# Kernel tuning notes

Hardware: AMD Instinct MI355X
Metric: run time of the kernel (lower is better)

## Reference

```python
import jax, jax.numpy as jnp
import numpy as np

B, P, ENC = 64, 196, 2048
H, A, E, V, T = 512, 512, 512, 10000, 20


def setup_inputs() -> dict:
    key = jax.random.key(0)
    ks = jax.random.split(key, 24)
    s = 0.02
    inp = {
        "encoder_out": jax.random.normal(ks[0], (B, P, ENC), jnp.float32),
        "captions": jax.random.randint(ks[1], (B, T), 0, V),
        "lengths": jnp.sort(jax.random.randint(ks[2], (B,), 5, T + 1))[::-1].at[0].set(T).astype(jnp.int32),
        # Attention
        "enc_att_w": jax.random.normal(ks[3], (A, ENC)) * s,
        "enc_att_b": jnp.zeros((A,)),
        "hid_att_w": jax.random.normal(ks[4], (A, H)) * s,
        "hid_att_b": jnp.zeros((A,)),
        "full_att_w": jax.random.normal(ks[5], (1, A)) * s,
        "full_att_b": jnp.zeros((1,)),
        # Embedding
        "embed_w": jax.random.uniform(ks[6], (V, E), minval=-0.1, maxval=0.1),
        # LSTMCell (input = embed + encoder -> E + ENC)
        "lstm_w_ih": jax.random.normal(ks[7], (4 * H, E + ENC)) * s,
        "lstm_w_hh": jax.random.normal(ks[8], (4 * H, H)) * s,
        "lstm_b_ih": jnp.zeros((4 * H,)),
        "lstm_b_hh": jnp.zeros((4 * H,)),
        # init hidden/cell from mean encoder features
        "init_h_w": jax.random.normal(ks[9], (H, ENC)) * s,
        "init_h_b": jnp.zeros((H,)),
        "init_c_w": jax.random.normal(ks[10], (H, ENC)) * s,
        "init_c_b": jnp.zeros((H,)),
        # gating
        "fbeta_w": jax.random.normal(ks[11], (ENC, H)) * s,
        "fbeta_b": jnp.zeros((ENC,)),
        # output fc
        "fc_w": jax.random.uniform(ks[12], (V, H), minval=-0.1, maxval=0.1),
        "fc_b": jnp.zeros((V,)),
    }
    return inp


def reference(encoder_out, captions, lengths,
              enc_att_w, enc_att_b, hid_att_w, hid_att_b, full_att_w, full_att_b,
              embed_w, lstm_w_ih, lstm_w_hh, lstm_b_ih, lstm_b_hh,
              init_h_w, init_h_b, init_c_w, init_c_b,
              fbeta_w, fbeta_b, fc_w, fc_b):
    emb = embed_w[captions]                      # [B, T, E]
    mean_enc = encoder_out.mean(axis=1)          # [B, ENC]
    h0 = mean_enc @ init_h_w.T + init_h_b
    c0 = mean_enc @ init_c_w.T + init_c_b
    # encoder attention projection is constant across timesteps
    att1 = encoder_out @ enc_att_w.T + enc_att_b  # [B, P, A]
    dec_len = lengths - 1                         # decode lengths per sample

    def step(carry, xs):
        h, c = carry
        emb_t, t = xs
        att2 = h @ hid_att_w.T + hid_att_b                     # [B, A]
        e = jax.nn.relu(att1 + att2[:, None, :]) @ full_att_w[0] + full_att_b[0]  # [B, P]
        alpha = jax.nn.softmax(e, axis=1)                       # [B, P]
        awe = jnp.einsum('bpe,bp->be', encoder_out, alpha)      # [B, ENC]
        gate = jax.nn.sigmoid(h @ fbeta_w.T + fbeta_b)
        x = jnp.concatenate([emb_t, gate * awe], axis=1)        # [B, E+ENC]
        gates = x @ lstm_w_ih.T + lstm_b_ih + h @ lstm_w_hh.T + lstm_b_hh
        i, f, g, o = jnp.split(gates, 4, axis=1)
        c_new = jax.nn.sigmoid(f) * c + jax.nn.sigmoid(i) * jnp.tanh(g)
        h_new = jax.nn.sigmoid(o) * jnp.tanh(c_new)
        pred = h_new @ fc_w.T + fc_b                            # [B, V]
        active = (t < dec_len)[:, None]
        h = jnp.where(active, h_new, h)
        c = jnp.where(active, c_new, c)
        pred = jnp.where(active, pred, jnp.zeros_like(pred))
        alpha = jnp.where(active, alpha, jnp.zeros_like(alpha))
        return (h, c), (pred, alpha)

    Tm1 = emb.shape[1] - 1
    ts = jnp.arange(Tm1)
    emb_seq = jnp.transpose(emb[:, :Tm1], (1, 0, 2))            # [T-1, B, E]
    (_, _), (preds, alphas) = jax.lax.scan(step, (h0, c0), (emb_seq, ts))
    predictions = jnp.transpose(preds, (1, 0, 2))               # [B, T-1, V]
    alphas = jnp.transpose(alphas, (1, 0, 2))                   # [B, T-1, P]
    return predictions, alphas
```

## Files before the change

kernel.cpp:

```cpp
#include <hip/hip_runtime.h>
#include <hip/hip_bf16.h>

typedef short short8  __attribute__((ext_vector_type(8)));
typedef float floatx4 __attribute__((ext_vector_type(4)));
typedef int   int4v   __attribute__((ext_vector_type(4)));

constexpr int BB = 64, PP = 196, CENC = 2048, HH = 512, AA = 512, EE = 512;
constexpr int VV = 10000, TT = 20, TM1 = 19;
constexpr int NCAT = 4608;

__device__ __forceinline__ float bf2f(short u) {
    union { unsigned u; float f; } v; v.u = ((unsigned)(unsigned short)u) << 16; return v.f;
}
__device__ __forceinline__ short f2bf(float f) {
    union { float f; unsigned u; } v; v.f = f;
    unsigned r = v.u + 0x7FFF + ((v.u >> 16) & 1);
    return (short)(r >> 16);
}

#define GLL(gp, lp) __builtin_amdgcn_global_load_lds( \
    (const __attribute__((address_space(1))) void*)(gp), \
    (__attribute__((address_space(3))) void*)(lp), 16, 0, 0)

__global__ __launch_bounds__(256)
void kPrepW(const float* __restrict__ encw_s, const float* __restrict__ haw,
            const float* __restrict__ fbw, const float* __restrict__ whh,
            const float* __restrict__ wih, const float* __restrict__ fcw,
            const float* __restrict__ hab, const float* __restrict__ fbb,
            const float* __restrict__ bih, const float* __restrict__ bhh,
            short* __restrict__ encw_d, short* __restrict__ wcat_d,
            short* __restrict__ wihe_d, short* __restrict__ wihm_d,
            short* __restrict__ fc_d, float* __restrict__ biascat,
            float* __restrict__ biasg)
{
    long e = ((long)blockIdx.x * 256 + threadIdx.x) * 8;
    const float* sp = nullptr; short* dp = nullptr; long de = 0;
    if (e < 1048576)       { sp = &encw_s[e]; dp = encw_d; de = e; }
    else if (e < 3407872)  { long u = e - 1048576; long row = u >> 9, col = u & 511;
                             sp = (row < 512) ? &haw[row * 512 + col]
                                : (row < 2560) ? &fbw[(row - 512) * 512 + col]
                                               : &whh[(row - 2560) * 512 + col];
                             dp = wcat_d; de = u; }
    else if (e < 7602176)  { long u = e - 3407872; long row = u >> 11, col = u & 2047;
                             sp = &wih[row * 2560 + 512 + col]; dp = wihe_d; de = u; }
    else if (e < 8650752)  { long u = e - 7602176; long row = u >> 9, col = u & 511;
                             sp = &wih[row * 2560 + col]; dp = wihm_d; de = u; }
    else if (e < 13770752) { long u = e - 8650752; sp = &fcw[u]; dp = fc_d; de = u; }
    else if (e < 13775360) { long u = e - 13770752;
                             for (int j = 0; j < 8; ++j) { long w = u + j;
                                 biascat[w] = (w < 512) ? hab[w] : ((w < 2560) ? fbb[w - 512] : 0.f); }
                             return; }
    else if (e < 13777408) { long u = e - 13775360;
                             for (int j = 0; j < 8; ++j) biasg[u + j] = bih[u + j] + bhh[u + j];
                             return; }
    else return;
    union { short s[8]; int4v v; } u8;
    #pragma unroll
    for (int j = 0; j < 8; ++j) u8.s[j] = f2bf(sp[j]);
    *reinterpret_cast<int4v*>(&dp[de]) = u8.v;
}

template<int FULL>
__global__ __launch_bounds__(256)
void kMeanEnc(const float* __restrict__ enc, short* __restrict__ enc16,
              float* __restrict__ meanP)
{
    int b = blockIdx.x, kc = blockIdx.y, pz = blockIdx.z;
    int k = kc * 256 + threadIdx.x;
    const float* eb = &enc[((size_t)b * PP + pz * 28) * CENC + k];
    short* ob = &enc16[((size_t)b * PP + pz * 28) * CENC + k];
    float s0 = 0, s1 = 0, s2 = 0, s3 = 0;
    for (int p = 0; p < 28; p += 4) {
        float v0 = eb[(size_t)(p + 0) * CENC], v1 = eb[(size_t)(p + 1) * CENC];
        float v2 = eb[(size_t)(p + 2) * CENC], v3 = eb[(size_t)(p + 3) * CENC];
        s0 += v0; s1 += v1; s2 += v2; s3 += v3;
        if (FULL) {
            ob[(size_t)(p + 0) * CENC] = f2bf(v0); ob[(size_t)(p + 1) * CENC] = f2bf(v1);
            ob[(size_t)(p + 2) * CENC] = f2bf(v2); ob[(size_t)(p + 3) * CENC] = f2bf(v3);
        }
    }
    meanP[((size_t)pz * 64 + b) * 2048 + k] = (s0 + s1) + (s2 + s3);
}

__global__ __launch_bounds__(256)
void kEmbGather(const float* __restrict__ embw, const int* __restrict__ captions,
                short* __restrict__ embA)
{
    long e = ((long)blockIdx.x * 256 + threadIdx.x) * 8;
    int r = (int)(e >> 9), j = (int)(e & 511);
    int t = r >> 6, b = r & 63;
    int tok = captions[b * TT + t];
    const float* sp = &embw[(size_t)tok * EE + j];
    union { short s[8]; int4v v; } u8;
    #pragma unroll
    for (int q = 0; q < 8; ++q) u8.s[q] = f2bf(sp[q]);
    *reinterpret_cast<int4v*>(&embA[e]) = u8.v;
}

template<int AOP, int WOP, int EOP, int SWZ>
__global__ __launch_bounds__(256)
void kGemm(const void* __restrict__ Ap, int lda, const short* __restrict__ W, int ldw,
           const float* __restrict__ bias, int Ntot,
           float* __restrict__ outF, int ldc, short* __restrict__ outB,
           int nk, const int* __restrict__ lengths)
{
    __shared__ short As[64 * 64];
    __shared__ short Ws[64 * 64];
    int nb, mb, kz;
    if (SWZ == 0) { nb = blockIdx.x; mb = blockIdx.y; kz = blockIdx.z; }
    else if (SWZ == 1) {
        int j = blockIdx.x;
        if (j < 1536) { mb = (j >> 6) * 8 + (j & 7); nb = (j >> 3) & 7; }
        else          { int u = j - 1536; mb = 192 + (u >> 3); nb = u & 7; }
        kz = 0;
    } else {
        int j = blockIdx.x; int c = j & 7, s = j >> 3;
        mb = s % 19; int u = s / 19; nb = 8 * u + c; kz = 0;
        if (nb * 64 >= Ntot) return;
    }
    const int tid = threadIdx.x;
    const int m0 = mb * 64, n0 = nb * 64, k0 = kz * nk * 64;
    const int w = tid >> 6, l = tid & 63;
    floatx4 acc[4] = {};

    for (int ks = 0; ks < nk; ++ks) {
        int kt = k0 + ks * 64;
        if (AOP == 0) {
            const short* A = (const short*)Ap;
            #pragma unroll
            for (int i = 0; i < 2; ++i) {
                int ii = w * 2 + i;
                int row = ii * 8 + (l >> 3);
                int cg = l & 7;
                const short* gp = &A[(size_t)(m0 + row) * lda + kt + ((cg ^ (row & 7)) << 3)];
                GLL(gp, &As[ii * 512]);
            }
        } else {
            const float* A = (const float*)Ap;
            #pragma unroll
            for (int i = 0; i < 2; ++i) {
                int s = tid + i * 256, row = s >> 3, cg = s & 7;
                const float* sp = &A[(size_t)(m0 + row) * lda + kt + cg * 8];
                float4 a = *reinterpret_cast<const float4*>(sp);
                float4 b = *reinterpret_cast<const float4*>(sp + 4);
                union { short s[8]; int4v v; } u8;
                u8.s[0]=f2bf(a.x); u8.s[1]=f2bf(a.y); u8.s[2]=f2bf(a.z); u8.s[3]=f2bf(a.w);
                u8.s[4]=f2bf(b.x); u8.s[5]=f2bf(b.y); u8.s[6]=f2bf(b.z); u8.s[7]=f2bf(b.w);
                *reinterpret_cast<int4v*>(&As[row * 64 + ((cg ^ (row & 7)) << 3)]) = u8.v;
            }
        }
        #pragma unroll
        for (int i = 0; i < 2; ++i) {
            int ii = w * 2 + i;
            int r = ii * 8 + (l >> 3);
            int cg = l & 7;
            int wr;
            if (WOP == 1) wr = 512 * (r >> 4) + 16 * nb + (r & 15);
            else          wr = n0 + r;
            if (WOP == 1 || wr < Ntot) {
                const short* gp = &W[(size_t)wr * ldw + kt + ((cg ^ (r & 7)) << 3)];
                GLL(gp, &Ws[ii * 512]);
            }
        }
        __syncthreads();
        #pragma unroll
        for (int kc = 0; kc < 2; ++kc) {
            int arow = 16 * w + (l & 15);
            int cg = 4 * kc + (l >> 4);
            short8 af = *reinterpret_cast<const short8*>(&As[arow * 64 + ((cg ^ (arow & 7)) << 3)]);
            #pragma unroll
            for (int q = 0; q < 4; ++q) {
                int wrow = 16 * q + (l & 15);
                short8 wf = *reinterpret_cast<const short8*>(&Ws[wrow * 64 + ((cg ^ (wrow & 7)) << 3)]);
                acc[q] = __builtin_amdgcn_mfma_f32_16x16x32_bf16(af, wf, acc[q], 0, 0, 0);
            }
        }
        __syncthreads();
    }
    int l4 = l >> 4, l15 = l & 15;
    #pragma unroll
    for (int q = 0; q < 4; ++q) {
        #pragma unroll
        for (int j = 0; j < 4; ++j) {
            int m = m0 + 16 * w + 4 * l4 + j;
            int n = n0 + 16 * q + l15;
            float val = acc[q][j];
            if (EOP == 0) {
                outF[(size_t)m * ldc + n] = val + bias[n];
            } else if (EOP == 1) {
                outB[(size_t)m * ldc + n] = f2bf(val + bias[n]);
            } else if (EOP == 2) {
                if (n < Ntot) {
                    int b = m & 63, tt = m >> 6;
                    bool act = tt < (lengths[b] - 1);
                    outF[((size_t)b * TM1 + tt) * VV + n] = act ? (val + bias[n]) : 0.f;
                }
            } else {
                int col = 512 * q + (n0 >> 2) + l15;
                int mloc = m - m0;
                outF[((size_t)kz * 64 + mloc) * 2048 + col] = val;
            }
        }
    }
}

__global__ __launch_bounds__(256)
void gemmInit(const float* __restrict__ meanP, const float* __restrict__ W1,
              const float* __restrict__ W2, float* __restrict__ C)
{
    __shared__ __align__(16) float As_[32][64];
    __shared__ __align__(16) float Ws_[32][64];
    const int tid = threadIdx.x;
    const int n0 = blockIdx.x * 64, kz = blockIdx.z, k0 = kz * 512;
    const int ty = tid >> 4, tx = tid & 15;
    float acc[4][4] = {};
    for (int kt = k0; kt < k0 + 512; kt += 32) {
        #pragma unroll
        for (int i = 0; i < 2; ++i) {
            int idx = tid + i * 256, row = idx >> 3, c4 = (idx & 7) * 4;
            float4 v = make_float4(0.f, 0.f, 0.f, 0.f);
            #pragma unroll
            for (int pz = 0; pz < 7; ++pz) {
                float4 u = *reinterpret_cast<const float4*>(
                    &meanP[((size_t)pz * 64 + row) * CENC + kt + c4]);
                v.x += u.x; v.y += u.y; v.z += u.z; v.w += u.w;
            }
            const float inv = 1.0f / PP;
            As_[c4 + 0][row] = v.x * inv; As_[c4 + 1][row] = v.y * inv;
            As_[c4 + 2][row] = v.z * inv; As_[c4 + 3][row] = v.w * inv;
        }
        #pragma unroll
        for (int i = 0; i < 2; ++i) {
            int idx = tid + i * 256, row = idx >> 3, c4 = (idx & 7) * 4;
            int n = n0 + row;
            const float* wr = (n < 512) ? &W1[(size_t)n * CENC + kt + c4]
                                        : &W2[(size_t)(n - 512) * CENC + kt + c4];
            float4 v = *reinterpret_cast<const float4*>(wr);
            Ws_[c4 + 0][row] = v.x; Ws_[c4 + 1][row] = v.y; Ws_[c4 + 2][row] = v.z; Ws_[c4 + 3][row] = v.w;
        }
        __syncthreads();
        #pragma unroll
        for (int kk = 0; kk < 32; ++kk) {
            float av[4], bv[4];
            *reinterpret_cast<float4*>(av) = *reinterpret_cast<const float4*>(&As_[kk][ty * 4]);
            *reinterpret_cast<float4*>(bv) = *reinterpret_cast<const float4*>(&Ws_[kk][tx * 4]);
            #pragma unroll
            for (int ii = 0; ii < 4; ++ii)
                #pragma unroll
                for (int jj = 0; jj < 4; ++jj)
                    acc[ii][jj] = fmaf(av[ii], bv[jj], acc[ii][jj]);
        }
        __syncthreads();
    }
    #pragma unroll
    for (int ii = 0; ii < 4; ++ii)
        #pragma unroll
        for (int jj = 0; jj < 4; ++jj)
            C[((size_t)kz * 64 + ty * 4 + ii) * 1024 + n0 + tx * 4 + jj] = acc[ii][jj];
}

__global__ __launch_bounds__(256)
void kReduceHC(const float* __restrict__ Pc, const float* __restrict__ hb,
               const float* __restrict__ cb, float* __restrict__ hc,
               short* __restrict__ h16)
{
    int b = blockIdx.x, tid = threadIdx.x;
    for (int j = tid; j < 1024; j += 256) {
        float s = Pc[((size_t)0 * BB + b) * 1024 + j] + Pc[((size_t)1 * BB + b) * 1024 + j]
                + Pc[((size_t)2 * BB + b) * 1024 + j] + Pc[((size_t)3 * BB + b) * 1024 + j];
        s += (j < 512) ? hb[j] : cb[j - 512];
        hc[b * 1024 + j] = s;
        if (j < 512) h16[b * 512 + j] = f2bf(s);
    }
}

__global__ __launch_bounds__(256)
void kStepB(const short* __restrict__ att1, const float* __restrict__ P3h,
            const float* __restrict__ faw, const float* __restrict__ fab,
            const int* __restrict__ lengths, float* __restrict__ alpha,
            float* __restrict__ alpha_out, int t)
{
    int b = blockIdx.x, tid = threadIdx.x;
    __shared__ float att2s[512];
    __shared__ float fw[512];
    __shared__ float es[PP];
    __shared__ float red[8];
    for (int a = tid; a < 512; a += 256) { att2s[a] = P3h[b * NCAT + a]; fw[a] = faw[a]; }
    __syncthreads();
    int wv = tid >> 6, lane = tid & 63;
    for (int p = wv; p < PP; p += 4) {
        short8 v = *reinterpret_cast<const short8*>(&att1[((size_t)b * PP + p) * 512 + lane * 8]);
        float s = 0.f;
        #pragma unroll
        for (int j = 0; j < 8; ++j) {
            float x = bf2f(v[j]) + att2s[lane * 8 + j];
            s += fmaxf(x, 0.f) * fw[lane * 8 + j];
        }
        #pragma unroll
        for (int off = 32; off > 0; off >>= 1) s += __shfl_down(s, off, 64);
        if (lane == 0) es[p] = s + fab[0];
    }
    __syncthreads();
    float m = -1e30f;
    for (int p = tid; p < PP; p += 256) m = fmaxf(m, es[p]);
    #pragma unroll
    for (int off = 32; off > 0; off >>= 1) m = fmaxf(m, __shfl_down(m, off, 64));
    if (lane == 0) red[wv] = m;
    __syncthreads();
    m = fmaxf(fmaxf(red[0], red[1]), fmaxf(red[2], red[3]));
    float ssum = 0.f;
    for (int p = tid; p < PP; p += 256) { float ev = __expf(es[p] - m); es[p] = ev; ssum += ev; }
    #pragma unroll
    for (int off = 32; off > 0; off >>= 1) ssum += __shfl_down(ssum, off, 64);
    if (lane == 0) red[4 + wv] = ssum;
    __syncthreads();
    float inv = 1.f / (red[4] + red[5] + red[6] + red[7]);
    bool active = t < (lengths[b] - 1);
    for (int p = tid; p < PP; p += 256) {
        float al = es[p] * inv;
        alpha[b * PP + p] = al;
        alpha_out[((size_t)b * TM1 + t) * PP + p] = active ? al : 0.f;
    }
}

template<int BF>
__global__ __launch_bounds__(256)
void kStepC(const void* __restrict__ encp, const float* __restrict__ alpha,
            const float* __restrict__ P3h, short* __restrict__ x16)
{
    int b = blockIdx.x, kc = blockIdx.y, tid = threadIdx.x;
    __shared__ float al[PP];
    __shared__ float part[8][256];
    for (int p = tid; p < PP; p += 256) al[p] = alpha[b * PP + p];
    __syncthreads();
    if (BF == 1) {
        const short* enc16 = (const short*)encp;
        int g = tid & 31, prow = tid >> 5;
        int k0 = kc * 256 + g * 8;
        float acc[8] = {};
        for (int p = prow; p < PP; p += 8) {
            short8 v = *reinterpret_cast<const short8*>(&enc16[((size_t)b * PP + p) * CENC + k0]);
            float a_ = al[p];
            #pragma unroll
            for (int j = 0; j < 8; ++j) acc[j] = fmaf(bf2f(v[j]), a_, acc[j]);
        }
        *reinterpret_cast<float4*>(&part[prow][g * 8])     = make_float4(acc[0], acc[1], acc[2], acc[3]);
        *reinterpret_cast<float4*>(&part[prow][g * 8 + 4]) = make_float4(acc[4], acc[5], acc[6], acc[7]);
        __syncthreads();
        int c = tid;
        float awe = 0.f;
        #pragma unroll
        for (int pr = 0; pr < 8; ++pr) awe += part[pr][c];
        int k = kc * 256 + c;
        float gate = 1.f / (1.f + __expf(-P3h[b * NCAT + 512 + k]));
        x16[(size_t)b * CENC + k] = f2bf(gate * awe);
    } else {
        const float* enc = (const float*)encp;
        int g = tid & 63, prow = tid >> 6;
        int k0 = kc * 256 + g * 4;
        float acc[4] = {};
        for (int p = prow; p < PP; p += 4) {
            float4 v = *reinterpret_cast<const float4*>(&enc[((size_t)b * PP + p) * CENC + k0]);
            float a_ = al[p];
            acc[0] = fmaf(v.x, a_, acc[0]); acc[1] = fmaf(v.y, a_, acc[1]);
            acc[2] = fmaf(v.z, a_, acc[2]); acc[3] = fmaf(v.w, a_, acc[3]);
        }
        *reinterpret_cast<float4*>(&part[prow][g * 4]) = make_float4(acc[0], acc[1], acc[2], acc[3]);
        __syncthreads();
        int c = tid;
        float awe = part[0][c] + part[1][c] + part[2][c] + part[3][c];
        int k = kc * 256 + c;
        float gate = 1.f / (1.f + __expf(-P3h[b * NCAT + 512 + k]));
        x16[(size_t)b * CENC + k] = f2bf(gate * awe);
    }
}

__global__ __launch_bounds__(256)
void kStepD2(const float* __restrict__ Pg, const float* __restrict__ gates_emb,
             const float* __restrict__ P3h, float* __restrict__ hc,
             short* __restrict__ h16, short* __restrict__ allH, int t)
{
    int b = blockIdx.x, tid = threadIdx.x;
    for (int d = tid; d < 512; d += 256) {
        float g4[4];
        #pragma unroll
        for (int q = 0; q < 4; ++q) {
            int col = q * 512 + d;
            float s = gates_emb[((size_t)t * 64 + b) * 2048 + col] + P3h[b * NCAT + 2560 + col];
            #pragma unroll
            for (int kz = 0; kz < 4; ++kz) s += Pg[((size_t)kz * 64 + b) * 2048 + col];
            g4[q] = s;
        }
        float i_ = 1.f / (1.f + __expf(-g4[0]));
        float f_ = 1.f / (1.f + __expf(-g4[1]));
        float g_ = tanhf(g4[2]);
        float o_ = 1.f / (1.f + __expf(-g4[3]));
        float c_new = f_ * hc[b * 1024 + 512 + d] + i_ * g_;
        float h_new = o_ * tanhf(c_new);
        hc[b * 1024 + 512 + d] = c_new;
        hc[b * 1024 + d] = h_new;
        short hb = f2bf(h_new);
        h16[b * 512 + d] = hb;
        allH[((size_t)t * 64 + b) * 512 + d] = hb;
    }
}

extern "C" void kernel_launch(void* const* d_in, const int* in_sizes, int n_in,
                              void* d_out, int out_size, void* d_ws, size_t ws_size,
                              hipStream_t stream)
{
    const float* enc        = (const float*)d_in[0];
    const int*   captions   = (const int*)d_in[1];
    const int*   lengths    = (const int*)d_in[2];
    const float* enc_att_w  = (const float*)d_in[3];
    const float* enc_att_b  = (const float*)d_in[4];
    const float* hid_att_w  = (const float*)d_in[5];
    const float* hid_att_b  = (const float*)d_in[6];
    const float* full_att_w = (const float*)d_in[7];
    const float* full_att_b = (const float*)d_in[8];
    const float* embw       = (const float*)d_in[9];
    const float* w_ih       = (const float*)d_in[10];
    const float* w_hh       = (const float*)d_in[11];
    const float* b_ih       = (const float*)d_in[12];
    const float* b_hh       = (const float*)d_in[13];
    const float* init_h_w   = (const float*)d_in[14];
    const float* init_h_b   = (const float*)d_in[15];
    const float* init_c_w   = (const float*)d_in[16];
    const float* init_c_b   = (const float*)d_in[17];
    const float* fbeta_w    = (const float*)d_in[18];
    const float* fbeta_b    = (const float*)d_in[19];
    const float* fc_w       = (const float*)d_in[20];
    const float* fc_b       = (const float*)d_in[21];

    float* out_pred  = (float*)d_out;
    float* out_alpha = out_pred + (size_t)BB * TM1 * VV;

    char* pr = (char*)d_out;
    short* att1_16   = (short*)pr;  pr += 12845056;
    float* gates_emb = (float*)pr;  pr += 9961472;
    short* wcat16    = (short*)pr;  pr += 4718592;
    short* wihe16    = (short*)pr;  pr += 8388608;
    float* biascat   = (float*)pr;  pr += 18432;
    float* P3h       = (float*)pr;  pr += 1179648;
    float* Pg        = (float*)pr;  pr += 2097152;
    short* embA      = (short*)pr;  pr += 1245184;
    short* wihm16    = (short*)pr;  pr += 2097152;
    short* encw16    = (short*)pr;  pr += 2097152;
    float* biasg     = (float*)pr;  pr += 8192;
    float* meanP     = (float*)pr;  pr += 3670016;
    float* hcP       = (float*)pr;  pr += 1048576;

    char* wp = (char*)d_ws;
    float* hc    = (float*)wp;  wp += 262144;
    short* h16   = (short*)wp;  wp += 65536;
    short* x16   = (short*)wp;  wp += 262144;
    float* alpha = (float*)wp;  wp += 50176;
    short* fc16  = (short*)wp;  wp += 10240000;
    short* allH  = (short*)wp;  wp += 1245184;
    short* enc16 = (short*)wp;  wp += 51380224;
    const bool full = ((size_t)(wp - (char*)d_ws) <= ws_size);

    kPrepW<<<6728, 256, 0, stream>>>(enc_att_w, hid_att_w, fbeta_w, w_hh, w_ih, fc_w,
                                     hid_att_b, fbeta_b, b_ih, b_hh,
                                     encw16, wcat16, wihe16, wihm16, fc16, biascat, biasg);
    if (full) kMeanEnc<1><<<dim3(64, 8, 7), 256, 0, stream>>>(enc, enc16, meanP);
    else      kMeanEnc<0><<<dim3(64, 8, 7), 256, 0, stream>>>(enc, enc16, meanP);
    kEmbGather<<<304, 256, 0, stream>>>(embw, captions, embA);
    gemmInit<<<dim3(16, 1, 4), 256, 0, stream>>>(meanP, init_h_w, init_c_w, hcP);
    kReduceHC<<<64, 256, 0, stream>>>(hcP, init_h_b, init_c_b, hc, h16);

    if (full)
        kGemm<0, 0, 1, 1><<<1568, 256, 0, stream>>>(enc16, CENC, encw16, CENC,
            enc_att_b, 512, nullptr, 512, att1_16, 32, nullptr);
    else
        kGemm<1, 0, 1, 1><<<1568, 256, 0, stream>>>(enc, CENC, encw16, CENC,
            enc_att_b, 512, nullptr, 512, att1_16, 32, nullptr);

    kGemm<0, 0, 0, 0><<<dim3(32, 19, 1), 256, 0, stream>>>(embA, 512, wihm16, 512,
        biasg, 2048, gates_emb, 2048, nullptr, 8, nullptr);

    for (int t = 0; t < TM1; ++t) {
        kGemm<0, 0, 0, 0><<<dim3(72, 1, 1), 256, 0, stream>>>(h16, 512, wcat16, 512,
            biascat, NCAT, P3h, NCAT, nullptr, 8, nullptr);

        kStepB<<<64, 256, 0, stream>>>(att1_16, P3h, full_att_w, full_att_b,
                                       lengths, alpha, out_alpha, t);

        if (full) kStepC<1><<<dim3(64, 8), 256, 0, stream>>>(enc16, alpha, P3h, x16);
        else      kStepC<0><<<dim3(64, 8), 256, 0, stream>>>(enc, alpha, P3h, x16);

        kGemm<0, 1, 4, 0><<<dim3(32, 1, 4), 256, 0, stream>>>(x16, CENC, wihe16, CENC,
            nullptr, 2048, Pg, 2048, nullptr, 8, nullptr);

        kStepD2<<<64, 256, 0, stream>>>(Pg, gates_emb, P3h, hc, h16, allH, t);
    }

    kGemm<0, 0, 2, 2><<<3040, 256, 0, stream>>>(allH, 512, fc16, 512,
        fc_b, VV, out_pred, VV, nullptr, 8, lengths);
}
```

Before: 1.334 ms.

## Fuse attention softmax into context kernel and move init GEMM to MFMA

```diff
diff --git a/kernel.cpp b/kernel.cpp
--- a/kernel.cpp
+++ b/kernel.cpp
@@ -26,12 +26,15 @@
 void kPrepW(const float* __restrict__ encw_s, const float* __restrict__ haw,
             const float* __restrict__ fbw, const float* __restrict__ whh,
             const float* __restrict__ wih, const float* __restrict__ fcw,
+            const float* __restrict__ ihw, const float* __restrict__ icw,
             const float* __restrict__ hab, const float* __restrict__ fbb,
             const float* __restrict__ bih, const float* __restrict__ bhh,
+            const float* __restrict__ ihb, const float* __restrict__ icb,
             short* __restrict__ encw_d, short* __restrict__ wcat_d,
             short* __restrict__ wihe_d, short* __restrict__ wihm_d,
-            short* __restrict__ fc_d, float* __restrict__ biascat,
-            float* __restrict__ biasg)
+            short* __restrict__ fc_d, short* __restrict__ initW_d,
+            float* __restrict__ biascat, float* __restrict__ biasg,
+            float* __restrict__ biasInit)
 {
     long e = ((long)blockIdx.x * 256 + threadIdx.x) * 8;
     const float* sp = nullptr; short* dp = nullptr; long de = 0;
@@ -46,12 +49,19 @@
     else if (e < 8650752)  { long u = e - 7602176; long row = u >> 9, col = u & 511;
                              sp = &wih[row * 2560 + col]; dp = wihm_d; de = u; }
     else if (e < 13770752) { long u = e - 8650752; sp = &fcw[u]; dp = fc_d; de = u; }
-    else if (e < 13775360) { long u = e - 13770752;
+    else if (e < 15867904) { long u = e - 13770752;
+                             sp = (u < 1048576) ? &ihw[u] : &icw[u - 1048576];
+                             dp = initW_d; de = u; }
+    else if (e < 15872512) { long u = e - 15867904;
                              for (int j = 0; j < 8; ++j) { long w = u + j;
                                  biascat[w] = (w < 512) ? hab[w] : ((w < 2560) ? fbb[w - 512] : 0.f); }
                              return; }
-    else if (e < 13777408) { long u = e - 13775360;
+    else if (e < 15874560) { long u = e - 15872512;
                              for (int j = 0; j < 8; ++j) biasg[u + j] = bih[u + j] + bhh[u + j];
+                             return; }
+    else if (e < 15875584) { long u = e - 15874560;
+                             for (int j = 0; j < 8; ++j) { long w = u + j;
+                                 biasInit[w] = (w < 512) ? ihb[w] : icb[w - 512]; }
                              return; }
     else return;
     union { short s[8]; int4v v; } u8;
@@ -80,6 +90,22 @@
         }
     }
     meanP[((size_t)pz * 64 + b) * 2048 + k] = (s0 + s1) + (s2 + s3);
+}
+
+__global__ __launch_bounds__(256)
+void kReduceMean(const float* __restrict__ meanP, short* __restrict__ mean16)
+{
+    int b = blockIdx.x, c0 = threadIdx.x * 8;
+    const float inv = 1.0f / PP;
+    union { short s[8]; int4v v; } u8;
+    #pragma unroll
+    for (int j = 0; j < 8; ++j) {
+        float s = 0.f;
+        #pragma unroll
+        for (int pz = 0; pz < 7; ++pz) s += meanP[((size_t)pz * 64 + b) * 2048 + c0 + j];
+        u8.s[j] = f2bf(s * inv);
+    }
+    *reinterpret_cast<int4v*>(&mean16[b * 2048 + c0]) = u8.v;
 }
 
 __global__ __launch_bounds__(256)
@@ -195,6 +221,9 @@
                     bool act = tt < (lengths[b] - 1);
                     outF[((size_t)b * TM1 + tt) * VV + n] = act ? (val + bias[n]) : 0.f;
                 }
+            } else if (EOP == 3) {
+                int mloc = m - m0;
+                outF[((size_t)kz * 64 + mloc) * ldc + n] = val;
             } else {
                 int col = 512 * q + (n0 >> 2) + l15;
                 int mloc = m - m0;
@@ -205,88 +234,38 @@
 }
 
 __global__ __launch_bounds__(256)
-void gemmInit(const float* __restrict__ meanP, const float* __restrict__ W1,
-              const float* __restrict__ W2, float* __restrict__ C)
-{
-    __shared__ __align__(16) float As_[32][64];
-    __shared__ __align__(16) float Ws_[32][64];
-    const int tid = threadIdx.x;
-    const int n0 = blockIdx.x * 64, kz = blockIdx.z, k0 = kz * 512;
-    const int ty = tid >> 4, tx = tid & 15;
-    float acc[4][4] = {};
-    for (int kt = k0; kt < k0 + 512; kt += 32) {
-        #pragma unroll
-        for (int i = 0; i < 2; ++i) {
-            int idx = tid + i * 256, row = idx >> 3, c4 = (idx & 7) * 4;
-            float4 v = make_float4(0.f, 0.f, 0.f, 0.f);
-            #pragma unroll
-            for (int pz = 0; pz < 7; ++pz) {
-                float4 u = *reinterpret_cast<const float4*>(
-                    &meanP[((size_t)pz * 64 + row) * CENC + kt + c4]);
-                v.x += u.x; v.y += u.y; v.z += u.z; v.w += u.w;
-            }
-            const float inv = 1.0f / PP;
-            As_[c4 + 0][row] = v.x * inv; As_[c4 + 1][row] = v.y * inv;
-            As_[c4 + 2][row] = v.z * inv; As_[c4 + 3][row] = v.w * inv;
-        }
-        #pragma unroll
-        for (int i = 0; i < 2; ++i) {
-            int idx = tid + i * 256, row = idx >> 3, c4 = (idx & 7) * 4;
-            int n = n0 + row;
-            const float* wr = (n < 512) ? &W1[(size_t)n * CENC + kt + c4]
-                                        : &W2[(size_t)(n - 512) * CENC + kt + c4];
-            float4 v = *reinterpret_cast<const float4*>(wr);
-            Ws_[c4 + 0][row] = v.x; Ws_[c4 + 1][row] = v.y; Ws_[c4 + 2][row] = v.z; Ws_[c4 + 3][row] = v.w;
-        }
-        __syncthreads();
-        #pragma unroll
-        for (int kk = 0; kk < 32; ++kk) {
-            float av[4], bv[4];
-            *reinterpret_cast<float4*>(av) = *reinterpret_cast<const float4*>(&As_[kk][ty * 4]);
-            *reinterpret_cast<float4*>(bv) = *reinterpret_cast<const float4*>(&Ws_[kk][tx * 4]);
-            #pragma unroll
-            for (int ii = 0; ii < 4; ++ii)
-                #pragma unroll
-                for (int jj = 0; jj < 4; ++jj)
-                    acc[ii][jj] = fmaf(av[ii], bv[jj], acc[ii][jj]);
-        }
-        __syncthreads();
-    }
-    #pragma unroll
-    for (int ii = 0; ii < 4; ++ii)
-        #pragma unroll
-        for (int jj = 0; jj < 4; ++jj)
-            C[((size_t)kz * 64 + ty * 4 + ii) * 1024 + n0 + tx * 4 + jj] = acc[ii][jj];
-}
-
-__global__ __launch_bounds__(256)
-void kReduceHC(const float* __restrict__ Pc, const float* __restrict__ hb,
-               const float* __restrict__ cb, float* __restrict__ hc,
-               short* __restrict__ h16)
+void kReduceHC(const float* __restrict__ Pc, const float* __restrict__ biasInit,
+               float* __restrict__ hc, short* __restrict__ h16)
 {
     int b = blockIdx.x, tid = threadIdx.x;
     for (int j = tid; j < 1024; j += 256) {
         float s = Pc[((size_t)0 * BB + b) * 1024 + j] + Pc[((size_t)1 * BB + b) * 1024 + j]
                 + Pc[((size_t)2 * BB + b) * 1024 + j] + Pc[((size_t)3 * BB + b) * 1024 + j];
-        s += (j < 512) ? hb[j] : cb[j - 512];
+        s += biasInit[j];
         hc[b * 1024 + j] = s;
         if (j < 512) h16[b * 512 + j] = f2bf(s);
     }
 }
 
-__global__ __launch_bounds__(256)
-void kStepB(const short* __restrict__ att1, const float* __restrict__ P3h,
-            const float* __restrict__ faw, const float* __restrict__ fab,
-            const int* __restrict__ lengths, float* __restrict__ alpha,
-            float* __restrict__ alpha_out, int t)
-{
-    int b = blockIdx.x, tid = threadIdx.x;
+template<int FULL>
+__global__ __launch_bounds__(256)
+void kStepBC(const short* __restrict__ att1, const float* __restrict__ P3h,
+             const float* __restrict__ faw, const float* __restrict__ fab,
+             const int* __restrict__ lengths, const void* __restrict__ encp,
+             short* __restrict__ x16, float* __restrict__ alpha_out, int t)
+{
+    int blk = blockIdx.x, tid = threadIdx.x;
+    int b = blk & 63, kc = blk >> 6;
     __shared__ float att2s[512];
     __shared__ float fw[512];
     __shared__ float es[PP];
+    __shared__ float alps[PP];
     __shared__ float red[8];
+    __shared__ float part[8][256];
+
     for (int a = tid; a < 512; a += 256) { att2s[a] = P3h[b * NCAT + a]; fw[a] = faw[a]; }
     __syncthreads();
+
     int wv = tid >> 6, lane = tid & 63;
     for (int p = wv; p < PP; p += 4) {
         short8 v = *reinterpret_cast<const short8*>(&att1[((size_t)b * PP + p) * 512 + lane * 8]);
@@ -318,29 +297,20 @@
     bool active = t < (lengths[b] - 1);
     for (int p = tid; p < PP; p += 256) {
         float al = es[p] * inv;
-        alpha[b * PP + p] = al;
-        alpha_out[((size_t)b * TM1 + t) * PP + p] = active ? al : 0.f;
-    }
-}
-
-template<int BF>
-__global__ __launch_bounds__(256)
-void kStepC(const void* __restrict__ encp, const float* __restrict__ alpha,
-            const float* __restrict__ P3h, short* __restrict__ x16)
-{
-    int b = blockIdx.x, kc = blockIdx.y, tid = threadIdx.x;
-    __shared__ float al[PP];
-    __shared__ float part[8][256];
-    for (int p = tid; p < PP; p += 256) al[p] = alpha[b * PP + p];
+        alps[p] = al;
+        if (kc == 0)
+            alpha_out[((size_t)b * TM1 + t) * PP + p] = active ? al : 0.f;
+    }
     __syncthreads();
-    if (BF == 1) {
+
+    if (FULL) {
         const short* enc16 = (const short*)encp;
         int g = tid & 31, prow = tid >> 5;
         int k0 = kc * 256 + g * 8;
         float acc[8] = {};
         for (int p = prow; p < PP; p += 8) {
             short8 v = *reinterpret_cast<const short8*>(&enc16[((size_t)b * PP + p) * CENC + k0]);
-            float a_ = al[p];
+            float a_ = alps[p];
             #pragma unroll
             for (int j = 0; j < 8; ++j) acc[j] = fmaf(bf2f(v[j]), a_, acc[j]);
         }
@@ -361,7 +331,7 @@
         float acc[4] = {};
         for (int p = prow; p < PP; p += 4) {
             float4 v = *reinterpret_cast<const float4*>(&enc[((size_t)b * PP + p) * CENC + k0]);
-            float a_ = al[p];
+            float a_ = alps[p];
             acc[0] = fmaf(v.x, a_, acc[0]); acc[1] = fmaf(v.y, a_, acc[1]);
             acc[2] = fmaf(v.z, a_, acc[2]); acc[3] = fmaf(v.w, a_, acc[3]);
         }
@@ -448,26 +418,34 @@
     short* encw16    = (short*)pr;  pr += 2097152;
     float* biasg     = (float*)pr;  pr += 8192;
     float* meanP     = (float*)pr;  pr += 3670016;
-    float* hcP       = (float*)pr;  pr += 1048576;
+    short* mean16    = (short*)pr;  pr += 262144;
+
+    short* initW16  = (short*)gates_emb;
+    float* biasInit = (float*)((char*)gates_emb + 4194304);
+    float* hcP      = P3h;
 
     char* wp = (char*)d_ws;
     float* hc    = (float*)wp;  wp += 262144;
     short* h16   = (short*)wp;  wp += 65536;
     short* x16   = (short*)wp;  wp += 262144;
-    float* alpha = (float*)wp;  wp += 50176;
     short* fc16  = (short*)wp;  wp += 10240000;
     short* allH  = (short*)wp;  wp += 1245184;
     short* enc16 = (short*)wp;  wp += 51380224;
     const bool full = ((size_t)(wp - (char*)d_ws) <= ws_size);
 
-    kPrepW<<<6728, 256, 0, stream>>>(enc_att_w, hid_att_w, fbeta_w, w_hh, w_ih, fc_w,
-                                     hid_att_b, fbeta_b, b_ih, b_hh,
-                                     encw16, wcat16, wihe16, wihm16, fc16, biascat, biasg);
+    kPrepW<<<7752, 256, 0, stream>>>(enc_att_w, hid_att_w, fbeta_w, w_hh, w_ih, fc_w,
+                                     init_h_w, init_c_w,
+                                     hid_att_b, fbeta_b, b_ih, b_hh, init_h_b, init_c_b,
+                                     encw16, wcat16, wihe16, wihm16, fc16, initW16,
+                                     biascat, biasg, biasInit);
     if (full) kMeanEnc<1><<<dim3(64, 8, 7), 256, 0, stream>>>(enc, enc16, meanP);
     else      kMeanEnc<0><<<dim3(64, 8, 7), 256, 0, stream>>>(enc, enc16, meanP);
     kEmbGather<<<304, 256, 0, stream>>>(embw, captions, embA);
-    gemmInit<<<dim3(16, 1, 4), 256, 0, stream>>>(meanP, init_h_w, init_c_w, hcP);
-    kReduceHC<<<64, 256, 0, stream>>>(hcP, init_h_b, init_c_b, hc, h16);
+    kReduceMean<<<64, 256, 0, stream>>>(meanP, mean16);
+
+    kGemm<0, 0, 3, 0><<<dim3(16, 1, 4), 256, 0, stream>>>(mean16, CENC, initW16, CENC,
+        nullptr, 1024, hcP, 1024, nullptr, 8, nullptr);
+    kReduceHC<<<64, 256, 0, stream>>>(hcP, biasInit, hc, h16);
 
     if (full)
         kGemm<0, 0, 1, 1><<<1568, 256, 0, stream>>>(enc16, CENC, encw16, CENC,
@@ -483,11 +461,10 @@
         kGemm<0, 0, 0, 0><<<dim3(72, 1, 1), 256, 0, stream>>>(h16, 512, wcat16, 512,
             biascat, NCAT, P3h, NCAT, nullptr, 8, nullptr);
 
-        kStepB<<<64, 256, 0, stream>>>(att1_16, P3h, full_att_w, full_att_b,
-                                       lengths, alpha, out_alpha, t);
-
-        if (full) kStepC<1><<<dim3(64, 8), 256, 0, stream>>>(enc16, alpha, P3h, x16);
-        else      kStepC<0><<<dim3(64, 8), 256, 0, stream>>>(enc, alpha, P3h, x16);
+        if (full) kStepBC<1><<<512, 256, 0, stream>>>(att1_16, P3h, full_att_w,
+            full_att_b, lengths, enc16, x16, out_alpha, t);
+        else      kStepBC<0><<<512, 256, 0, stream>>>(att1_16, P3h, full_att_w,
+            full_att_b, lengths, enc, x16, out_alpha, t);
 
         kGemm<0, 1, 4, 0><<<dim3(32, 1, 4), 256, 0, stream>>>(x16, CENC, wihe16, CENC,
             nullptr, 2048, Pg, 2048, nullptr, 8, nullptr);
```

After: 1.228 ms, median of 2. 7.9% less time.
